# Performance work log

Measured on AMD Instinct MI355X. Metric: run time of the kernel, lower is better.

The kernel has to match this reference:

```python
import jax, jax.numpy as jnp
import numpy as np

B, H, W, C = 8, 64, 64, 256
NH, WS, SS = 8, 8, 4
HD = C // NH          # head dim 32
N = WS * WS           # 64 tokens per window
NW = (H // WS) * (W // WS)  # 64 windows
MLP = 4 * C


def _rel_index():
    ch = np.arange(WS)
    coords = np.stack(np.meshgrid(ch, ch, indexing='ij')).reshape(2, -1)  # [2, N]
    rel = (coords[:, :, None] - coords[:, None, :]).transpose(1, 2, 0)   # [N, N, 2]
    rel[:, :, 0] += WS - 1
    rel[:, :, 1] += WS - 1
    rel[:, :, 0] *= 2 * WS - 1
    return jnp.asarray(rel.sum(-1))  # [N, N] indices into table

REL_IDX = _rel_index()


def _attn_mask():
    # standard Swin shifted-window mask: [nW, N, N] with 0 / -100
    img = np.zeros((H, W))
    slices = (slice(0, -WS), slice(-WS, -SS), slice(-SS, None))
    cnt = 0
    for hs in slices:
        for ws_ in slices:
            img[hs, ws_] = cnt
            cnt += 1
    m = img.reshape(H // WS, WS, W // WS, WS).transpose(0, 2, 1, 3).reshape(-1, N)
    diff = m[:, None, :] - m[:, :, None]
    return jnp.asarray(np.where(diff != 0, -100.0, 0.0).astype(np.float32))

MASK = _attn_mask()


def setup_inputs() -> dict:
    key = jax.random.key(0)
    ks = jax.random.split(key, 8)
    s = 0.02
    return {
        'hidden_states': jax.random.normal(ks[0], (B, H * W, C), jnp.float32),
        'ln1_g': jnp.ones((C,), jnp.float32),
        'ln1_b': jnp.zeros((C,), jnp.float32),
        'wq': jax.random.normal(ks[1], (C, C), jnp.float32) * s,
        'bq': jnp.zeros((C,), jnp.float32),
        'wk': jax.random.normal(ks[2], (C, C), jnp.float32) * s,
        'bk': jnp.zeros((C,), jnp.float32),
        'wv': jax.random.normal(ks[3], (C, C), jnp.float32) * s,
        'bv': jnp.zeros((C,), jnp.float32),
        'rel_table': jax.random.normal(ks[4], ((2 * WS - 1) ** 2, NH), jnp.float32) * s,
        'wo': jax.random.normal(ks[5], (C, C), jnp.float32) * s,
        'bo': jnp.zeros((C,), jnp.float32),
        'ln2_g': jnp.ones((C,), jnp.float32),
        'ln2_b': jnp.zeros((C,), jnp.float32),
        'w1': jax.random.normal(ks[6], (MLP, C), jnp.float32) * s,
        'b1': jnp.zeros((MLP,), jnp.float32),
        'w2': jax.random.normal(ks[7], (C, MLP), jnp.float32) * s,
        'b2': jnp.zeros((C,), jnp.float32),
    }


def _ln(x, g, b):
    mu = x.mean(-1, keepdims=True)
    var = x.var(-1, keepdims=True)
    return (x - mu) * jax.lax.rsqrt(var + 1e-5) * g + b


def reference(hidden_states, ln1_g, ln1_b, wq, bq, wk, bk, wv, bv, rel_table,
              wo, bo, ln2_g, ln2_b, w1, b1, w2, b2):
    shortcut = hidden_states
    x = _ln(hidden_states, ln1_g, ln1_b).reshape(B, H, W, C)
    # cyclic shift
    x = jnp.roll(x, (-SS, -SS), axis=(1, 2))
    # window partition -> [B*nW, N, C]
    xw = x.reshape(B, H // WS, WS, W // WS, WS, C).transpose(0, 1, 3, 2, 4, 5).reshape(-1, N, C)
    q = (xw @ wq.T + bq).reshape(-1, N, NH, HD).transpose(0, 2, 1, 3)
    k = (xw @ wk.T + bk).reshape(-1, N, NH, HD).transpose(0, 2, 1, 3)
    v = (xw @ wv.T + bv).reshape(-1, N, NH, HD).transpose(0, 2, 1, 3)
    scores = jnp.einsum('bhnd,bhmd->bhnm', q, k) / np.float32(np.sqrt(HD))
    bias = rel_table[REL_IDX]                 # [N, N, NH] gathered bias
    scores = scores + bias.transpose(2, 0, 1)[None]
    scores = scores.reshape(B, NW, NH, N, N) + MASK[None, :, None]
    probs = jax.nn.softmax(scores, axis=-1).reshape(-1, NH, N, N)
    ctx = jnp.einsum('bhnm,bhmd->bnhd', probs, v).reshape(-1, N, C)
    attn_out = ctx @ wo.T + bo                # SelfOutput dense
    # window reverse + reverse shift
    x = attn_out.reshape(B, H // WS, W // WS, WS, WS, C).transpose(0, 1, 3, 2, 4, 5).reshape(B, H, W, C)
    x = jnp.roll(x, (SS, SS), axis=(1, 2)).reshape(B, H * W, C)
    hidden = shortcut + x
    y = _ln(hidden, ln2_g, ln2_b)
    y = jax.nn.gelu(y @ w1.T + b1, approximate=False) @ w2.T + b2
    return hidden + y
```

## Files before the change

kernel.cpp:

```cpp
#include <hip/hip_runtime.h>
#include <hip/hip_bf16.h>
#include <math.h>

__device__ __forceinline__ unsigned short f2bf(float f) {
    union { float f; unsigned u; } c; c.f = f;
    unsigned r = c.u + 0x7fffu + ((c.u >> 16) & 1u);
    return (unsigned short)(r >> 16);
}
__device__ __forceinline__ float bfu(unsigned short u) {
    union { unsigned x; float f; } c; c.x = ((unsigned)u) << 16; return c.f;
}
__device__ __forceinline__ float gelu_t(float x) {
    float z = x * (1.59576912f + 0.07135481f * x * x);
    return x / (1.0f + __expf(-z));
}

typedef __bf16 bf16x8_t __attribute__((ext_vector_type(8)));
typedef float  f32x4_t  __attribute__((ext_vector_type(4)));
typedef unsigned short u16x8 __attribute__((ext_vector_type(8)));

#define AS1 __attribute__((address_space(1)))
#define AS3 __attribute__((address_space(3)))
__device__ __forceinline__ void g2lds16(const void* g, void* l) {
    __builtin_amdgcn_global_load_lds((const AS1 unsigned int*)g, (AS3 unsigned int*)l, 16, 0, 0);
}

__global__ void cvt_all(const float* __restrict__ wq, const float* __restrict__ wk,
                        const float* __restrict__ wv, const float* __restrict__ wo,
                        const float* __restrict__ w1, const float* __restrict__ w2,
                        const float* __restrict__ ln2g,
                        unsigned short* __restrict__ wqkv_b, unsigned short* __restrict__ wo_b,
                        unsigned short* __restrict__ w1_b, unsigned short* __restrict__ w2_b) {
    int i = blockIdx.x * 256 + threadIdx.x;
    const float* src; unsigned short* dst; int base; int isw1 = 0;
    if (i < 16384)       { src = wq; dst = wqkv_b;          base = 0; }
    else if (i < 32768)  { src = wk; dst = wqkv_b + 65536;  base = 16384; }
    else if (i < 49152)  { src = wv; dst = wqkv_b + 131072; base = 32768; }
    else if (i < 65536)  { src = wo; dst = wo_b;            base = 49152; }
    else if (i < 131072) { src = w1; dst = w1_b;            base = 65536; isw1 = 1; }
    else                 { src = w2; dst = w2_b;            base = 131072; }
    int j = (i - base) * 4;
    float4 v = *(const float4*)(src + j);
    if (isw1) {
        float4 g = *(const float4*)(ln2g + (j & 255));
        v.x *= g.x; v.y *= g.y; v.z *= g.z; v.w *= g.w;
    }
    ushort4 o = { f2bf(v.x), f2bf(v.y), f2bf(v.z), f2bf(v.w) };
    *(ushort4*)(dst + j) = o;
}

__global__ void prep_mlp(const float* __restrict__ w1, const float* __restrict__ ln2g,
                         const float* __restrict__ ln2b, const float* __restrict__ b1,
                         float* __restrict__ s1, float* __restrict__ b1p) {
    int n = blockIdx.x * 256 + threadIdx.x;
    const float* wr = w1 + (size_t)n * 256;
    float ss = 0.f, sb = 0.f;
    #pragma unroll 4
    for (int k = 0; k < 256; k += 4) {
        float4 w = *(const float4*)(wr + k);
        float4 g = *(const float4*)(ln2g + k);
        float4 b = *(const float4*)(ln2b + k);
        ss += w.x * g.x + w.y * g.y + w.z * g.z + w.w * g.w;
        sb += w.x * b.x + w.y * b.y + w.z * b.z + w.w * b.w;
    }
    s1[n] = ss;
    b1p[n] = b1[n] + sb;
}

template<int GATHER, int BF16IN>
__global__ void ln_kernel(const void* __restrict__ xv, const float* __restrict__ g,
                          const float* __restrict__ b, unsigned short* __restrict__ out) {
    int row  = blockIdx.x * 4 + (threadIdx.x >> 6);
    int lane = threadIdx.x & 63;
    int src;
    if (GATHER) {
        int bb = row >> 12;
        int rem = row & 4095;
        int winid = rem >> 6, tok = rem & 63;
        int wi = winid >> 3, wj = winid & 7;
        int ii = tok >> 3,  jj = tok & 7;
        int hh = (wi * 8 + ii + 4) & 63;
        int ww = (wj * 8 + jj + 4) & 63;
        src = (bb << 12) + hh * 64 + ww;
    } else {
        src = row;
    }
    float4 v;
    if (BF16IN) {
        ushort4 u = *(const ushort4*)((const unsigned short*)xv + (size_t)src * 256 + lane * 4);
        v.x = bfu(u.x); v.y = bfu(u.y); v.z = bfu(u.z); v.w = bfu(u.w);
    } else {
        v = *(const float4*)((const float*)xv + (size_t)src * 256 + lane * 4);
    }
    float s  = v.x + v.y + v.z + v.w;
    float s2 = v.x*v.x + v.y*v.y + v.z*v.z + v.w*v.w;
    #pragma unroll
    for (int off = 32; off > 0; off >>= 1) {
        s  += __shfl_xor(s,  off, 64);
        s2 += __shfl_xor(s2, off, 64);
    }
    float mean = s * (1.0f / 256.0f);
    float var  = s2 * (1.0f / 256.0f) - mean * mean;
    float rstd = rsqrtf(var + 1e-5f);
    int c0 = lane * 4;
    float4 gg  = *(const float4*)(g + c0);
    float4 bb4 = *(const float4*)(b + c0);
    ushort4 o;
    o.x = f2bf((v.x - mean) * rstd * gg.x + bb4.x);
    o.y = f2bf((v.y - mean) * rstd * gg.y + bb4.y);
    o.z = f2bf((v.z - mean) * rstd * gg.z + bb4.z);
    o.w = f2bf((v.w - mean) * rstd * gg.w + bb4.w);
    *(ushort4*)(out + (size_t)row * 256 + c0) = o;
}

template<int MODE, int K>
__global__ __launch_bounds__(256, 4) void gemm_tile(
        const unsigned short* __restrict__ A,
        const unsigned short* __restrict__ Bw,
        const float* __restrict__ bias,
        int M, int N,
        unsigned short* __restrict__ obf,
        float* __restrict__ of32,
        const void* __restrict__ addp) {
    __shared__ __align__(16) char smem_raw[64 * 132 * 4];
    unsigned short* sm = (unsigned short*)smem_raw;
    float* cst = (float*)smem_raw;
    const int t = threadIdx.x;
    const int lane = t & 63, wave = t >> 6;
    const int m0 = blockIdx.x * 128, n0 = blockIdx.y * 128;
    const int wm = (wave >> 1) * 64, wn = (wave & 1) * 64;
    const int lr = lane & 15, kg = lane >> 4;

    f32x4_t acc[4][4];
    #pragma unroll
    for (int i = 0; i < 4; ++i)
        #pragma unroll
        for (int j = 0; j < 4; ++j) { acc[i][j][0]=0.f; acc[i][j][1]=0.f; acc[i][j][2]=0.f; acc[i][j][3]=0.f; }

    const unsigned short* ga = A  + (size_t)(m0 + (t >> 2)) * K + (t & 3) * 8;
    const unsigned short* gb = Bw + (size_t)(n0 + (t >> 2)) * K + (t & 3) * 8;
    unsigned short* lA = sm + t * 8;
    unsigned short* lB = sm + 4096 + t * 8;

    const int NT = K / 32;
    g2lds16(ga,                  lA);
    g2lds16(ga + (size_t)64 * K, lA + 2048);
    g2lds16(gb,                  lB);
    g2lds16(gb + (size_t)64 * K, lB + 2048);
    __syncthreads();

    #pragma unroll
    for (int k = 0; k < NT; ++k) {
        const int cur = k & 1;
        if (k + 1 < NT) {
            const int nx = cur ^ 1;
            const unsigned short* gA = ga + (k + 1) * 32;
            const unsigned short* gB = gb + (k + 1) * 32;
            g2lds16(gA,                  lA + nx * 8192);
            g2lds16(gA + (size_t)64 * K, lA + nx * 8192 + 2048);
            g2lds16(gB,                  lB + nx * 8192);
            g2lds16(gB + (size_t)64 * K, lB + nx * 8192 + 2048);
        }
        const unsigned short* Ab = sm + cur * 8192;
        const unsigned short* Bb = Ab + 4096;
        bf16x8_t af[4], bfr[4];
        #pragma unroll
        for (int i = 0; i < 4; ++i)
            af[i] = *(const bf16x8_t*)&Ab[(wm + i * 16 + lr) * 32 + kg * 8];
        #pragma unroll
        for (int j = 0; j < 4; ++j)
            bfr[j] = *(const bf16x8_t*)&Bb[(wn + j * 16 + lr) * 32 + kg * 8];
        #pragma unroll
        for (int i = 0; i < 4; ++i)
            #pragma unroll
            for (int j = 0; j < 4; ++j)
                acc[i][j] = __builtin_amdgcn_mfma_f32_16x16x32_bf16(af[i], bfr[j], acc[i][j], 0, 0, 0);
        __syncthreads();
    }

    #pragma unroll
    for (int pass = 0; pass < 2; ++pass) {
        __syncthreads();
        if ((wave >> 1) == pass) {
            float* cw = cst + (kg * 4) * 132 + wn + lr;
            #pragma unroll
            for (int i = 0; i < 4; ++i)
                #pragma unroll
                for (int j = 0; j < 4; ++j)
                    #pragma unroll
                    for (int e = 0; e < 4; ++e)
                        cw[(i * 16 + e) * 132 + j * 16] = acc[i][j][e];
        }
        __syncthreads();
        const int rr = t >> 4;
        const int ch = t & 15;
        if (MODE == 0) {
            #pragma unroll
            for (int c = 0; c < 4; ++c) {
                int r = rr + c * 16;
                int grow = m0 + pass * 64 + r;
                const float* cr = cst + r * 132 + ch * 8;
                const float* bp = bias + n0 + ch * 8;
                float4 a   = *(const float4*)(cr);
                float4 b4  = *(const float4*)(cr + 4);
                float4 ba  = *(const float4*)(bp);
                float4 bb4 = *(const float4*)(bp + 4);
                u16x8 o = { f2bf(a.x + ba.x),  f2bf(a.y + ba.y),  f2bf(a.z + ba.z),  f2bf(a.w + ba.w),
                            f2bf(b4.x + bb4.x), f2bf(b4.y + bb4.y), f2bf(b4.z + bb4.z), f2bf(b4.w + bb4.w) };
                *(u16x8*)(obf + (size_t)grow * N + n0 + ch * 8) = o;
            }
        } else {
            #pragma unroll
            for (int c = 0; c < 4; ++c) {
                int r = rr + c * 16;
                int grow = m0 + pass * 64 + r;
                int bb_ = grow >> 12, rem = grow & 4095;
                int winid = rem >> 6, tok = rem & 63;
                int wi = winid >> 3, wj = winid & 7;
                int ii = tok >> 3,  jj = tok & 7;
                int hh = (wi * 8 + ii + 4) & 63;
                int ww = (wj * 8 + jj + 4) & 63;
                size_t drow = (size_t)(bb_ << 12) + hh * 64 + ww;
                const float* cr = cst + r * 132 + ch * 8;
                const float* bp = bias + n0 + ch * 8;
                const float* res = (const float*)addp + drow * N + n0 + ch * 8;
                float4 a   = *(const float4*)(cr);
                float4 b4  = *(const float4*)(cr + 4);
                float4 ba  = *(const float4*)(bp);
                float4 bb4 = *(const float4*)(bp + 4);
                float4 ra  = *(const float4*)(res);
                float4 rb  = *(const float4*)(res + 4);
                u16x8 o = { f2bf(a.x + ba.x + ra.x),  f2bf(a.y + ba.y + ra.y),
                            f2bf(a.z + ba.z + ra.z),  f2bf(a.w + ba.w + ra.w),
                            f2bf(b4.x + bb4.x + rb.x), f2bf(b4.y + bb4.y + rb.y),
                            f2bf(b4.z + bb4.z + rb.z), f2bf(b4.w + bb4.w + rb.w) };
                *(u16x8*)(obf + drow * N + n0 + ch * 8) = o;
            }
        }
    }
}

__global__ __launch_bounds__(256, 1) void fused_mlp(
        const unsigned short* __restrict__ hb,
        const unsigned short* __restrict__ w1g,
        const unsigned short* __restrict__ w2b,
        const float* __restrict__ s1,
        const float* __restrict__ b1p,
        const float* __restrict__ b2,
        float* __restrict__ out) {
    extern __shared__ __align__(16) char sm[];
    unsigned short* w1c = (unsigned short*)sm;
    unsigned short* w2c = (unsigned short*)(sm + 32768);
    unsigned short* h1c = (unsigned short*)(sm + 65536);
    const int t = threadIdx.x, lane = t & 63, wave = t >> 6;
    const int lr = lane & 15, quad = lane >> 4;
    const size_t rowbase = (size_t)blockIdx.x * 128;

    const int xr = t >> 1, xh = t & 1;
    float s = 0.f, s2 = 0.f;
    {
        const unsigned short* xp = hb + (rowbase + xr) * 256 + xh * 128;
        u16x8 xf[16];
        #pragma unroll
        for (int f = 0; f < 16; ++f) {
            xf[f] = *(const u16x8*)(xp + f * 8);
            #pragma unroll
            for (int e = 0; e < 8; ++e) { float v = bfu(xf[f][e]); s += v; s2 += v * v; }
        }
        unsigned short* xt = (unsigned short*)sm;
        #pragma unroll
        for (int f = 0; f < 16; ++f) {
            int kk = xh * 4 + (f >> 2), kw = (f & 3) * 8;
            *(u16x8*)(xt + kk * 4096 + xr * 32 + kw) = xf[f];
        }
    }
    s  += __shfl_xor(s, 1, 64);
    s2 += __shfl_xor(s2, 1, 64);
    float mean = s * (1.0f / 256.0f);
    float var  = s2 * (1.0f / 256.0f) - mean * mean;
    float v_rst  = rsqrtf(var + 1e-5f);
    float v_murs = mean * v_rst;
    __syncthreads();

    bf16x8_t xa[2][8];
    {
        const unsigned short* xt = (const unsigned short*)sm;
        #pragma unroll
        for (int rs = 0; rs < 2; ++rs)
            #pragma unroll
            for (int kk = 0; kk < 8; ++kk)
                xa[rs][kk] = *(const bf16x8_t*)(xt + kk * 4096 + (wave * 32 + rs * 16 + lr) * 32 + quad * 8);
    }
    float murs[2][4], rstv[2][4];
    #pragma unroll
    for (int rs = 0; rs < 2; ++rs)
        #pragma unroll
        for (int e = 0; e < 4; ++e) {
            int srcl = 2 * (rs * 16 + quad * 4 + e);
            murs[rs][e] = __shfl(v_murs, srcl, 64);
            rstv[rs][e] = __shfl(v_rst,  srcl, 64);
        }
    __syncthreads();

    auto stage = [&](int c, int buf) {
        #pragma unroll
        for (int i = 0; i < 4; ++i) {
            int n1 = (t >> 2) & 31, kk1 = i * 2 + (t >> 7), kw = (t & 3) * 8;
            g2lds16(w1g + (size_t)(c * 32 + n1) * 256 + kk1 * 32 + kw,
                    w1c + buf * 8192 + i * 2048 + t * 8);
            int n2 = i * 64 + (t >> 2);
            g2lds16(w2b + (size_t)n2 * 1024 + c * 32 + kw,
                    w2c + buf * 8192 + i * 2048 + t * 8);
        }
    };
    stage(0, 0);

    f32x4_t zz[2][16];
    #pragma unroll
    for (int rs = 0; rs < 2; ++rs)
        #pragma unroll
        for (int cs = 0; cs < 16; ++cs) { zz[rs][cs][0]=0.f; zz[rs][cs][1]=0.f; zz[rs][cs][2]=0.f; zz[rs][cs][3]=0.f; }
    __syncthreads();

    unsigned short* H = h1c + wave * 1280;
    for (int c = 0; c < 32; ++c) {
        const int cur = c & 1;
        if (c + 1 < 32) stage(c + 1, cur ^ 1);
        const unsigned short* W1 = w1c + cur * 8192;
        const unsigned short* W2 = w2c + cur * 8192;
        f32x4_t a1[2][2];
        #pragma unroll
        for (int rs = 0; rs < 2; ++rs)
            #pragma unroll
            for (int ns = 0; ns < 2; ++ns) { a1[rs][ns][0]=0.f; a1[rs][ns][1]=0.f; a1[rs][ns][2]=0.f; a1[rs][ns][3]=0.f; }
        #pragma unroll
        for (int kk = 0; kk < 8; ++kk) {
            bf16x8_t b0 = *(const bf16x8_t*)&W1[kk * 1024 + lr * 32 + quad * 8];
            bf16x8_t b1f = *(const bf16x8_t*)&W1[kk * 1024 + (16 + lr) * 32 + quad * 8];
            a1[0][0] = __builtin_amdgcn_mfma_f32_16x16x32_bf16(xa[0][kk], b0,  a1[0][0], 0, 0, 0);
            a1[0][1] = __builtin_amdgcn_mfma_f32_16x16x32_bf16(xa[0][kk], b1f, a1[0][1], 0, 0, 0);
            a1[1][0] = __builtin_amdgcn_mfma_f32_16x16x32_bf16(xa[1][kk], b0,  a1[1][0], 0, 0, 0);
            a1[1][1] = __builtin_amdgcn_mfma_f32_16x16x32_bf16(xa[1][kk], b1f, a1[1][1], 0, 0, 0);
        }
        float s1v[2], b1v[2];
        #pragma unroll
        for (int ns = 0; ns < 2; ++ns) {
            int col = c * 32 + ns * 16 + lr;
            s1v[ns] = s1[col];
            b1v[ns] = b1p[col];
        }
        #pragma unroll
        for (int rs = 0; rs < 2; ++rs)
            #pragma unroll
            for (int ns = 0; ns < 2; ++ns)
                #pragma unroll
                for (int e = 0; e < 4; ++e) {
                    float h = rstv[rs][e] * a1[rs][ns][e] - murs[rs][e] * s1v[ns] + b1v[ns];
                    H[(rs * 16 + quad * 4 + e) * 40 + ns * 16 + lr] = f2bf(gelu_t(h));
                }
        __asm__ volatile("s_waitcnt lgkmcnt(0)" ::: "memory");
        bf16x8_t pa0 = *(const bf16x8_t*)&H[lr * 40 + quad * 8];
        bf16x8_t pa1 = *(const bf16x8_t*)&H[(16 + lr) * 40 + quad * 8];
        #pragma unroll
        for (int cs = 0; cs < 16; ++cs) {
            bf16x8_t vb = *(const bf16x8_t*)&W2[(cs * 16 + lr) * 32 + quad * 8];
            zz[0][cs] = __builtin_amdgcn_mfma_f32_16x16x32_bf16(pa0, vb, zz[0][cs], 0, 0, 0);
            zz[1][cs] = __builtin_amdgcn_mfma_f32_16x16x32_bf16(pa1, vb, zz[1][cs], 0, 0, 0);
        }
        __syncthreads();
    }

    float* cst = (float*)sm;
    #pragma unroll
    for (int pass = 0; pass < 2; ++pass) {
        __syncthreads();
        if ((wave >> 1) == pass) {
            #pragma unroll
            for (int rs = 0; rs < 2; ++rs)
                #pragma unroll
                for (int cs = 0; cs < 16; ++cs)
                    #pragma unroll
                    for (int e = 0; e < 4; ++e)
                        cst[((wave & 1) * 32 + rs * 16 + quad * 4 + e) * 260 + cs * 16 + lr] = zz[rs][cs][e];
        }
        __syncthreads();
        const int r = t >> 2, q = t & 3;
        size_t grow = rowbase + pass * 64 + r;
        const float* cr = cst + r * 260 + q * 64;
        const unsigned short* rp = hb + grow * 256 + q * 64;
        float* op = out + grow * 256 + q * 64;
        #pragma unroll
        for (int c4 = 0; c4 < 16; ++c4) {
            float4 a  = *(const float4*)(cr + c4 * 4);
            float4 bb = *(const float4*)(b2 + q * 64 + c4 * 4);
            ushort4 rv = *(const ushort4*)(rp + c4 * 4);
            float4 o = { a.x + bb.x + bfu(rv.x), a.y + bb.y + bfu(rv.y),
                         a.z + bb.z + bfu(rv.z), a.w + bb.w + bfu(rv.w) };
            *(float4*)(op + c4 * 4) = o;
        }
    }
}

#define PR 72
#define VR 72
__global__ void __launch_bounds__(256) attn_mfma(
        const unsigned short* __restrict__ qkv,
        const float* __restrict__ relt,
        unsigned short* __restrict__ ctx) {
    __shared__ float rs[1800];
    __shared__ unsigned short Pl[4][64 * PR];
    __shared__ unsigned short Vt[4][32 * VR];

    int t = threadIdx.x;
    int lane = t & 63, wave = t >> 6;
    for (int i = t; i < 1800; i += 256) rs[i] = relt[i];
    __syncthreads();

    int wh = blockIdx.x * 4 + wave;
    int wg = wh >> 3, h = wh & 7;
    int win = wg & 63;
    int ln = lane & 15, quad = lane >> 4;

    unsigned short* P = &Pl[wave][0];
    unsigned short* V = &Vt[wave][0];
    const unsigned short* base = qkv + (size_t)wg * 64 * 768 + h * 32;

    union BF8 { bf16x8_t v; unsigned short s[8]; };
    {
        const bf16x8_t* vp = (const bf16x8_t*)(base + (size_t)lane * 768 + 512);
        BF8 vv[4];
        #pragma unroll
        for (int c = 0; c < 4; ++c) vv[c].v = vp[c];
        #pragma unroll
        for (int c = 0; c < 4; ++c)
            #pragma unroll
            for (int e = 0; e < 8; ++e)
                V[(c * 8 + e) * VR + lane] = vv[c].s[e];
    }

    bf16x8_t qa[4], kb[4];
    #pragma unroll
    for (int i = 0; i < 4; ++i)
        qa[i] = *(const bf16x8_t*)(base + (size_t)(i * 16 + ln) * 768 + quad * 8);
    #pragma unroll
    for (int j = 0; j < 4; ++j)
        kb[j] = *(const bf16x8_t*)(base + (size_t)(j * 16 + ln) * 768 + 256 + quad * 8);

    f32x4_t acc[4][4];
    #pragma unroll
    for (int i = 0; i < 4; ++i)
        #pragma unroll
        for (int j = 0; j < 4; ++j) { acc[i][j][0]=0.f; acc[i][j][1]=0.f; acc[i][j][2]=0.f; acc[i][j][3]=0.f; }
    #pragma unroll
    for (int i = 0; i < 4; ++i)
        #pragma unroll
        for (int j = 0; j < 4; ++j)
            acc[i][j] = __builtin_amdgcn_mfma_f32_16x16x32_bf16(qa[i], kb[j], acc[i][j], 0, 0, 0);

    const float scale = 0.17677669529663687f;
    int wi = win >> 3, wj = win & 7;
    int mjv = ln & 7;
    int regm[4], mi[4];
    #pragma unroll
    for (int j = 0; j < 4; ++j) {
        mi[j] = j * 2 + (ln >> 3);
        int hm = wi * 8 + mi[j], wm = wj * 8 + mjv;
        regm[j] = (hm < 56 ? 0 : (hm < 60 ? 1 : 2)) * 3 + (wm < 56 ? 0 : (wm < 60 ? 1 : 2));
    }
    float inv[4][4];
    #pragma unroll
    for (int i = 0; i < 4; ++i) {
        #pragma unroll
        for (int e = 0; e < 4; ++e) {
            int q = i * 16 + quad * 4 + e;
            int ti = q >> 3, tj = q & 7;
            int hn = wi * 8 + ti, wn = wj * 8 + tj;
            int regn = (hn < 56 ? 0 : (hn < 60 ? 1 : 2)) * 3 + (wn < 56 ? 0 : (wn < 60 ? 1 : 2));
            float sum = 0.f;
            #pragma unroll
            for (int j = 0; j < 4; ++j) {
                float bv = rs[((ti - mi[j] + 7) * 15 + (tj - mjv + 7)) * 8 + h];
                float sv = acc[i][j][e] * scale + bv + (regm[j] != regn ? -100.f : 0.f);
                float p = __expf(sv);
                sum += p;
                P[q * PR + j * 16 + ln] = f2bf(p);
            }
            #pragma unroll
            for (int off = 1; off < 16; off <<= 1) sum += __shfl_xor(sum, off, 64);
            inv[i][e] = 1.0f / sum;
        }
    }
    __syncthreads();

    bf16x8_t vb[2][2];
    #pragma unroll
    for (int jd = 0; jd < 2; ++jd)
        #pragma unroll
        for (int kc = 0; kc < 2; ++kc)
            vb[jd][kc] = *(const bf16x8_t*)&V[(jd * 16 + ln) * VR + kc * 32 + quad * 8];
    f32x4_t occ[4][2];
    #pragma unroll
    for (int i = 0; i < 4; ++i)
        #pragma unroll
        for (int jd = 0; jd < 2; ++jd) { occ[i][jd][0]=0.f; occ[i][jd][1]=0.f; occ[i][jd][2]=0.f; occ[i][jd][3]=0.f; }
    #pragma unroll
    for (int i = 0; i < 4; ++i) {
        #pragma unroll
        for (int kc = 0; kc < 2; ++kc) {
            bf16x8_t pf = *(const bf16x8_t*)&P[(i * 16 + ln) * PR + kc * 32 + quad * 8];
            occ[i][0] = __builtin_amdgcn_mfma_f32_16x16x32_bf16(pf, vb[0][kc], occ[i][0], 0, 0, 0);
            occ[i][1] = __builtin_amdgcn_mfma_f32_16x16x32_bf16(pf, vb[1][kc], occ[i][1], 0, 0, 0);
        }
    }

    unsigned short* cbase = ctx + (size_t)wg * 64 * 256 + h * 32;
    #pragma unroll
    for (int i = 0; i < 4; ++i)
        #pragma unroll
        for (int e = 0; e < 4; ++e) {
            int q = i * 16 + quad * 4 + e;
            #pragma unroll
            for (int jd = 0; jd < 2; ++jd)
                cbase[(size_t)q * 256 + jd * 16 + ln] = f2bf(occ[i][jd][e] * inv[i][e]);
        }
}

extern "C" void kernel_launch(void* const* d_in, const int* in_sizes, int n_in,
                              void* d_out, int out_size, void* d_ws, size_t ws_size,
                              hipStream_t stream) {
    const float* hs   = (const float*)d_in[0];
    const float* ln1g = (const float*)d_in[1];
    const float* ln1b = (const float*)d_in[2];
    const float* wq   = (const float*)d_in[3];
    const float* bq   = (const float*)d_in[4];
    const float* wk   = (const float*)d_in[5];
    const float* bk   = (const float*)d_in[6];
    const float* wv   = (const float*)d_in[7];
    const float* bv   = (const float*)d_in[8];
    const float* relt = (const float*)d_in[9];
    const float* wo   = (const float*)d_in[10];
    const float* bo   = (const float*)d_in[11];
    const float* ln2g = (const float*)d_in[12];
    const float* ln2b = (const float*)d_in[13];
    const float* w1   = (const float*)d_in[14];
    const float* b1   = (const float*)d_in[15];
    const float* w2   = (const float*)d_in[16];
    const float* b2   = (const float*)d_in[17];
    float* out = (float*)d_out;

    const size_t NTOK = 32768;
    size_t off = 0;
    auto carve = [&](size_t bytes) { void* p = (char*)d_ws + off; off += (bytes + 255) & ~(size_t)255; return p; };
    unsigned short* wqkv_b = (unsigned short*)carve(768ull * 256 * 2);
    unsigned short* wo_b   = (unsigned short*)carve(65536ull * 2);
    unsigned short* w1_b   = (unsigned short*)carve(262144ull * 2);
    unsigned short* w2_b   = (unsigned short*)carve(262144ull * 2);
    float*          bqkv   = (float*)carve(768ull * 4);
    float*          s1w    = (float*)carve(1024ull * 4);
    float*          b1w    = (float*)carve(1024ull * 4);
    unsigned short* hiddenb= (unsigned short*)carve(NTOK * 256 * 2);
    unsigned short* xw     = (unsigned short*)carve(NTOK * 256 * 2);
    unsigned short* qkvb   = (unsigned short*)carve(NTOK * 768 * 2);
    unsigned short* cx     = (unsigned short*)carve(NTOK * 256 * 2);

    static bool attr_set = false;
    if (!attr_set) {
        hipFuncSetAttribute(reinterpret_cast<const void*>(fused_mlp),
                            hipFuncAttributeMaxDynamicSharedMemorySize, 75776);
        attr_set = true;
    }

    cvt_all<<<768, 256, 0, stream>>>(wq, wk, wv, wo, w1, w2, ln2g, wqkv_b, wo_b, w1_b, w2_b);
    prep_mlp<<<4, 256, 0, stream>>>(w1, ln2g, ln2b, b1, s1w, b1w);
    hipMemcpyAsync(bqkv,       bq, 256 * 4, hipMemcpyDeviceToDevice, stream);
    hipMemcpyAsync(bqkv + 256, bk, 256 * 4, hipMemcpyDeviceToDevice, stream);
    hipMemcpyAsync(bqkv + 512, bv, 256 * 4, hipMemcpyDeviceToDevice, stream);

    ln_kernel<1, 0><<<8192, 256, 0, stream>>>(hs, ln1g, ln1b, xw);

    gemm_tile<0, 256><<<dim3(256, 6), 256, 0, stream>>>(xw, wqkv_b, bqkv, 32768, 768, qkvb, nullptr, nullptr);

    attn_mfma<<<1024, 256, 0, stream>>>(qkvb, relt, cx);

    gemm_tile<2, 256><<<dim3(256, 2), 256, 0, stream>>>(cx, wo_b, bo, 32768, 256, hiddenb, nullptr, hs);

    fused_mlp<<<256, 256, 75776, stream>>>(hiddenb, w1_b, w2_b, s1w, b1w, b2, out);
}
```

Before: 285.8 us.

## Pre-pack weights into MFMA fragment order for contiguous LDS loads

The weight conversion kernel now writes the bf16 weights in a packed layout that matches the MFMA B-fragment order per 32-wide K step and per 16-row subtile. The GEMM and fused MLP kernels can then stage them with fully contiguous global-to-LDS copies and read fragments as lane*8 offsets, with no strided row addressing. The MLP's GELU intermediate buffer is also repacked into fragment order, dropping its padding and shrinking dynamic shared memory. The goal is fewer LDS bank conflicts and simpler address math. The packing index math must exactly match the consumer reads, which is a correctness risk.

Result: no change. 286.4 us (+0.2%).

```diff
diff --git a/kernel.cpp b/kernel.cpp
--- a/kernel.cpp
+++ b/kernel.cpp
@@ -29,24 +29,49 @@
                         const float* __restrict__ wv, const float* __restrict__ wo,
                         const float* __restrict__ w1, const float* __restrict__ w2,
                         const float* __restrict__ ln2g,
-                        unsigned short* __restrict__ wqkv_b, unsigned short* __restrict__ wo_b,
-                        unsigned short* __restrict__ w1_b, unsigned short* __restrict__ w2_b) {
-    int i = blockIdx.x * 256 + threadIdx.x;
-    const float* src; unsigned short* dst; int base; int isw1 = 0;
-    if (i < 16384)       { src = wq; dst = wqkv_b;          base = 0; }
-    else if (i < 32768)  { src = wk; dst = wqkv_b + 65536;  base = 16384; }
-    else if (i < 49152)  { src = wv; dst = wqkv_b + 131072; base = 32768; }
-    else if (i < 65536)  { src = wo; dst = wo_b;            base = 49152; }
-    else if (i < 131072) { src = w1; dst = w1_b;            base = 65536; isw1 = 1; }
-    else                 { src = w2; dst = w2_b;            base = 131072; }
-    int j = (i - base) * 4;
-    float4 v = *(const float4*)(src + j);
-    if (isw1) {
-        float4 g = *(const float4*)(ln2g + (j & 255));
-        v.x *= g.x; v.y *= g.y; v.z *= g.z; v.w *= g.w;
-    }
-    ushort4 o = { f2bf(v.x), f2bf(v.y), f2bf(v.z), f2bf(v.w) };
-    *(ushort4*)(dst + j) = o;
+                        unsigned short* __restrict__ qkvp, unsigned short* __restrict__ wop,
+                        unsigned short* __restrict__ w1p, unsigned short* __restrict__ w2p) {
+    int fid = blockIdx.x * 256 + threadIdx.x;
+    const float* src; unsigned short* dst; size_t oidx; int scale = 0; int k0 = 0;
+    if (fid < 24576) {
+        int n = fid >> 5, kf = fid & 31;
+        const float* w = (n < 256) ? wq : (n < 512 ? wk : wv);
+        src = w + (size_t)(n & 255) * 256 + kf * 8;
+        dst = qkvp;
+        oidx = (size_t)(((n >> 7) * 8 + (kf >> 2)) * 4096)
+             + ((n >> 4) & 7) * 512 + (kf & 3) * 128 + (n & 15) * 8;
+    } else if (fid < 32768) {
+        int fi = fid - 24576;
+        int n = fi >> 5, kf = fi & 31;
+        src = wo + (size_t)n * 256 + kf * 8;
+        dst = wop;
+        oidx = (size_t)(((n >> 7) * 8 + (kf >> 2)) * 4096)
+             + ((n >> 4) & 7) * 512 + (kf & 3) * 128 + (n & 15) * 8;
+    } else if (fid < 65536) {
+        int fi = fid - 32768;
+        int n = fi >> 5, kf = fi & 31;
+        src = w1 + (size_t)n * 256 + kf * 8;
+        dst = w1p; scale = 1; k0 = kf * 8;
+        oidx = (size_t)((n >> 5) * 8192) + (kf >> 2) * 1024 + ((n >> 4) & 1) * 512
+             + (kf & 3) * 128 + (n & 15) * 8;
+    } else {
+        int fi = fid - 65536;
+        int n = fi >> 7, kf = fi & 127;
+        src = w2 + (size_t)n * 1024 + kf * 8;
+        dst = w2p;
+        oidx = (size_t)((kf >> 2) * 8192) + (n >> 4) * 512 + (kf & 3) * 128 + (n & 15) * 8;
+    }
+    float4 a = *(const float4*)(src);
+    float4 b = *(const float4*)(src + 4);
+    if (scale) {
+        float4 g0 = *(const float4*)(ln2g + k0);
+        float4 g1 = *(const float4*)(ln2g + k0 + 4);
+        a.x *= g0.x; a.y *= g0.y; a.z *= g0.z; a.w *= g0.w;
+        b.x *= g1.x; b.y *= g1.y; b.z *= g1.z; b.w *= g1.w;
+    }
+    u16x8 o = { f2bf(a.x), f2bf(a.y), f2bf(a.z), f2bf(a.w),
+                f2bf(b.x), f2bf(b.y), f2bf(b.z), f2bf(b.w) };
+    *(u16x8*)(dst + oidx) = o;
 }
 
 __global__ void prep_mlp(const float* __restrict__ w1, const float* __restrict__ ln2g,
@@ -116,11 +141,10 @@
 template<int MODE, int K>
 __global__ __launch_bounds__(256, 4) void gemm_tile(
         const unsigned short* __restrict__ A,
-        const unsigned short* __restrict__ Bw,
+        const unsigned short* __restrict__ Bp,
         const float* __restrict__ bias,
         int M, int N,
         unsigned short* __restrict__ obf,
-        float* __restrict__ of32,
         const void* __restrict__ addp) {
     __shared__ __align__(16) char smem_raw[64 * 132 * 4];
     unsigned short* sm = (unsigned short*)smem_raw;
@@ -137,16 +161,16 @@
         #pragma unroll
         for (int j = 0; j < 4; ++j) { acc[i][j][0]=0.f; acc[i][j][1]=0.f; acc[i][j][2]=0.f; acc[i][j][3]=0.f; }
 
-    const unsigned short* ga = A  + (size_t)(m0 + (t >> 2)) * K + (t & 3) * 8;
-    const unsigned short* gb = Bw + (size_t)(n0 + (t >> 2)) * K + (t & 3) * 8;
+    const unsigned short* ga  = A  + (size_t)(m0 + (t >> 2)) * K + (t & 3) * 8;
+    const unsigned short* gbp = Bp + (size_t)blockIdx.y * (K / 32) * 4096 + t * 8;
     unsigned short* lA = sm + t * 8;
     unsigned short* lB = sm + 4096 + t * 8;
 
     const int NT = K / 32;
     g2lds16(ga,                  lA);
     g2lds16(ga + (size_t)64 * K, lA + 2048);
-    g2lds16(gb,                  lB);
-    g2lds16(gb + (size_t)64 * K, lB + 2048);
+    g2lds16(gbp,                 lB);
+    g2lds16(gbp + 2048,          lB + 2048);
     __syncthreads();
 
     #pragma unroll
@@ -154,12 +178,10 @@
         const int cur = k & 1;
         if (k + 1 < NT) {
             const int nx = cur ^ 1;
-            const unsigned short* gA = ga + (k + 1) * 32;
-            const unsigned short* gB = gb + (k + 1) * 32;
-            g2lds16(gA,                  lA + nx * 8192);
-            g2lds16(gA + (size_t)64 * K, lA + nx * 8192 + 2048);
-            g2lds16(gB,                  lB + nx * 8192);
-            g2lds16(gB + (size_t)64 * K, lB + nx * 8192 + 2048);
+            g2lds16(ga + (k + 1) * 32,                  lA + nx * 8192);
+            g2lds16(ga + (size_t)64 * K + (k + 1) * 32, lA + nx * 8192 + 2048);
+            g2lds16(gbp + (k + 1) * 4096,               lB + nx * 8192);
+            g2lds16(gbp + (k + 1) * 4096 + 2048,        lB + nx * 8192 + 2048);
         }
         const unsigned short* Ab = sm + cur * 8192;
         const unsigned short* Bb = Ab + 4096;
@@ -169,7 +191,7 @@
             af[i] = *(const bf16x8_t*)&Ab[(wm + i * 16 + lr) * 32 + kg * 8];
         #pragma unroll
         for (int j = 0; j < 4; ++j)
-            bfr[j] = *(const bf16x8_t*)&Bb[(wn + j * 16 + lr) * 32 + kg * 8];
+            bfr[j] = *(const bf16x8_t*)&Bb[(((wave & 1) * 4 + j) * 64 + lane) * 8];
         #pragma unroll
         for (int i = 0; i < 4; ++i)
             #pragma unroll
@@ -242,8 +264,8 @@
 
 __global__ __launch_bounds__(256, 1) void fused_mlp(
         const unsigned short* __restrict__ hb,
-        const unsigned short* __restrict__ w1g,
-        const unsigned short* __restrict__ w2b,
+        const unsigned short* __restrict__ w1p,
+        const unsigned short* __restrict__ w2p,
         const float* __restrict__ s1,
         const float* __restrict__ b1p,
         const float* __restrict__ b2,
@@ -305,12 +327,8 @@
     auto stage = [&](int c, int buf) {
         #pragma unroll
         for (int i = 0; i < 4; ++i) {
-            int n1 = (t >> 2) & 31, kk1 = i * 2 + (t >> 7), kw = (t & 3) * 8;
-            g2lds16(w1g + (size_t)(c * 32 + n1) * 256 + kk1 * 32 + kw,
-                    w1c + buf * 8192 + i * 2048 + t * 8);
-            int n2 = i * 64 + (t >> 2);
-            g2lds16(w2b + (size_t)n2 * 1024 + c * 32 + kw,
-                    w2c + buf * 8192 + i * 2048 + t * 8);
+            g2lds16(w1p + (size_t)c * 8192 + i * 2048 + t * 8, w1c + buf * 8192 + i * 2048 + t * 8);
+            g2lds16(w2p + (size_t)c * 8192 + i * 2048 + t * 8, w2c + buf * 8192 + i * 2048 + t * 8);
         }
     };
     stage(0, 0);
@@ -322,7 +340,7 @@
         for (int cs = 0; cs < 16; ++cs) { zz[rs][cs][0]=0.f; zz[rs][cs][1]=0.f; zz[rs][cs][2]=0.f; zz[rs][cs][3]=0.f; }
     __syncthreads();
 
-    unsigned short* H = h1c + wave * 1280;
+    unsigned short* H = h1c + wave * 1024;
     for (int c = 0; c < 32; ++c) {
         const int cur = c & 1;
         if (c + 1 < 32) stage(c + 1, cur ^ 1);
@@ -335,8 +353,8 @@
             for (int ns = 0; ns < 2; ++ns) { a1[rs][ns][0]=0.f; a1[rs][ns][1]=0.f; a1[rs][ns][2]=0.f; a1[rs][ns][3]=0.f; }
         #pragma unroll
         for (int kk = 0; kk < 8; ++kk) {
-            bf16x8_t b0 = *(const bf16x8_t*)&W1[kk * 1024 + lr * 32 + quad * 8];
-            bf16x8_t b1f = *(const bf16x8_t*)&W1[kk * 1024 + (16 + lr) * 32 + quad * 8];
+            bf16x8_t b0  = *(const bf16x8_t*)&W1[kk * 1024 + lane * 8];
+            bf16x8_t b1f = *(const bf16x8_t*)&W1[kk * 1024 + 512 + lane * 8];
             a1[0][0] = __builtin_amdgcn_mfma_f32_16x16x32_bf16(xa[0][kk], b0,  a1[0][0], 0, 0, 0);
             a1[0][1] = __builtin_amdgcn_mfma_f32_16x16x32_bf16(xa[0][kk], b1f, a1[0][1], 0, 0, 0);
             a1[1][0] = __builtin_amdgcn_mfma_f32_16x16x32_bf16(xa[1][kk], b0,  a1[1][0], 0, 0, 0);
@@ -356,14 +374,14 @@
                 #pragma unroll
                 for (int e = 0; e < 4; ++e) {
                     float h = rstv[rs][e] * a1[rs][ns][e] - murs[rs][e] * s1v[ns] + b1v[ns];
-                    H[(rs * 16 + quad * 4 + e) * 40 + ns * 16 + lr] = f2bf(gelu_t(h));
+                    H[(rs * 4 + ns * 2 + (lr >> 3)) * 128 + (quad * 4 + e) * 8 + (lr & 7)] = f2bf(gelu_t(h));
                 }
         __asm__ volatile("s_waitcnt lgkmcnt(0)" ::: "memory");
-        bf16x8_t pa0 = *(const bf16x8_t*)&H[lr * 40 + quad * 8];
-        bf16x8_t pa1 = *(const bf16x8_t*)&H[(16 + lr) * 40 + quad * 8];
+        bf16x8_t pa0 = *(const bf16x8_t*)&H[lane * 8];
+        bf16x8_t pa1 = *(const bf16x8_t*)&H[512 + lane * 8];
         #pragma unroll
         for (int cs = 0; cs < 16; ++cs) {
-            bf16x8_t vb = *(const bf16x8_t*)&W2[(cs * 16 + lr) * 32 + quad * 8];
+            bf16x8_t vb = *(const bf16x8_t*)&W2[cs * 512 + lane * 8];
             zz[0][cs] = __builtin_amdgcn_mfma_f32_16x16x32_bf16(pa0, vb, zz[0][cs], 0, 0, 0);
             zz[1][cs] = __builtin_amdgcn_mfma_f32_16x16x32_bf16(pa1, vb, zz[1][cs], 0, 0, 0);
         }
@@ -551,10 +569,10 @@
     const size_t NTOK = 32768;
     size_t off = 0;
     auto carve = [&](size_t bytes) { void* p = (char*)d_ws + off; off += (bytes + 255) & ~(size_t)255; return p; };
-    unsigned short* wqkv_b = (unsigned short*)carve(768ull * 256 * 2);
-    unsigned short* wo_b   = (unsigned short*)carve(65536ull * 2);
-    unsigned short* w1_b   = (unsigned short*)carve(262144ull * 2);
-    unsigned short* w2_b   = (unsigned short*)carve(262144ull * 2);
+    unsigned short* wqkv_p = (unsigned short*)carve(768ull * 256 * 2);
+    unsigned short* wo_p   = (unsigned short*)carve(65536ull * 2);
+    unsigned short* w1p    = (unsigned short*)carve(262144ull * 2);
+    unsigned short* w2p    = (unsigned short*)carve(262144ull * 2);
     float*          bqkv   = (float*)carve(768ull * 4);
     float*          s1w    = (float*)carve(1024ull * 4);
     float*          b1w    = (float*)carve(1024ull * 4);
@@ -566,11 +584,11 @@
     static bool attr_set = false;
     if (!attr_set) {
         hipFuncSetAttribute(reinterpret_cast<const void*>(fused_mlp),
-                            hipFuncAttributeMaxDynamicSharedMemorySize, 75776);
+                            hipFuncAttributeMaxDynamicSharedMemorySize, 73728);
         attr_set = true;
     }
 
-    cvt_all<<<768, 256, 0, stream>>>(wq, wk, wv, wo, w1, w2, ln2g, wqkv_b, wo_b, w1_b, w2_b);
+    cvt_all<<<384, 256, 0, stream>>>(wq, wk, wv, wo, w1, w2, ln2g, wqkv_p, wo_p, w1p, w2p);
     prep_mlp<<<4, 256, 0, stream>>>(w1, ln2g, ln2b, b1, s1w, b1w);
     hipMemcpyAsync(bqkv,       bq, 256 * 4, hipMemcpyDeviceToDevice, stream);
     hipMemcpyAsync(bqkv + 256, bk, 256 * 4, hipMemcpyDeviceToDevice, stream);
@@ -578,11 +596,11 @@
 
     ln_kernel<1, 0><<<8192, 256, 0, stream>>>(hs, ln1g, ln1b, xw);
 
-    gemm_tile<0, 256><<<dim3(256, 6), 256, 0, stream>>>(xw, wqkv_b, bqkv, 32768, 768, qkvb, nullptr, nullptr);
+    gemm_tile<0, 256><<<dim3(256, 6), 256, 0, stream>>>(xw, wqkv_p, bqkv, 32768, 768, qkvb, nullptr);
 
     attn_mfma<<<1024, 256, 0, stream>>>(qkvb, relt, cx);
 
-    gemm_tile<2, 256><<<dim3(256, 2), 256, 0, stream>>>(cx, wo_b, bo, 32768, 256, hiddenb, nullptr, hs);
-
-    fused_mlp<<<256, 256, 75776, stream>>>(hiddenb, w1_b, w2_b, s1w, b1w, b2, out);
-}
+    gemm_tile<2, 256><<<dim3(256, 2), 256, 0, stream>>>(cx, wo_p, bo, 32768, 256, hiddenb, hs);
+
+    fused_mlp<<<256, 256, 73728, stream>>>(hiddenb, w1p, w2p, s1w, b1w, b2, out);
+}
```
